# Optimization experiments

Hardware: AMD Instinct MI355X
Metric: run time of the kernel (lower is better)

Reference implementation:

```python
import jax, jax.numpy as jnp
import numpy as np

SIZE = 64          # node feature dim
T = 12             # num edge styles
N = 4000           # notes (nodes)
B = 1              # graph batch (torch branch requires B==1)
S2 = SIZE          # secondary_size == size (secondary_size=0 default)


def setup_inputs() -> dict:
    key = jax.random.key(0)
    ks = jax.random.split(key, 5)
    std_a = (2.0 / (S2 + S2)) ** 0.5
    std_b = (2.0 / (SIZE + S2)) ** 0.5
    std_c = (2.0 / (SIZE * T + S2)) ** 0.5
    x = jax.random.normal(ks[0], (B, N, SIZE), jnp.float32)
    # dense per-edge-type adjacency; scaled so repeated propagation stays bounded
    edge_matrix = jax.random.normal(ks[1], (T, N, N), jnp.float32) / np.float32(np.sqrt(N))
    ba = jnp.zeros((T, SIZE), jnp.float32)
    bw = jnp.zeros((3 * S2,), jnp.float32)
    wz_wr_wh = std_c * jax.random.normal(ks[2], (T, SIZE, 3 * S2), jnp.float32)
    uz_ur = std_b * jax.random.normal(ks[3], (SIZE, 2 * S2), jnp.float32)
    uh = std_a * jax.random.normal(ks[4], (S2, S2), jnp.float32)
    return dict(x=x, edge_matrix=edge_matrix, ba=ba, bw=bw,
                wz_wr_wh=wz_wr_wh, uz_ur=uz_ur, uh=uh, iteration=10)


def reference(x, edge_matrix, ba, bw, wz_wr_wh, uz_ur, uh, iteration):
    h = x  # [B, N, S]
    for _ in range(iteration):
        # per-edge-type propagation: edge_matrix[t].T @ h  -> [B, T, N, S]
        act = jnp.einsum('tnm,bns->btms', edge_matrix, h) + ba[None, :, None, :]
        # fused z/r/h projection per edge type: [B, T, N, 3*S2]
        awzrh = jnp.einsum('btms,tsk->btmk', act, wz_wr_wh) + bw
        awz, awr, awh = jnp.split(awzrh, 3, axis=-1)
        awz = awz.sum(1)  # sum over edge types -> [B, N, S2]
        awr = awr.sum(1)
        awh = awh.sum(1)
        uzr = h @ uz_ur                      # [B, N, 2*S2]
        uz, ur = jnp.split(uzr, 2, axis=-1)
        z = jax.nn.sigmoid(awz + uz)
        r = jax.nn.sigmoid(awr + ur)
        hh = jnp.tanh(awh + (r * h) @ uh)    # secondary_size == size branch
        h = (1.0 - z) * h + z * hh
    return h
```

## Files before the change

kernel.cpp:

```cpp
#include <hip/hip_runtime.h>
#include <stdint.h>

#define NN 4000
#define SD 64
#define TT 12
#define NITER 10
#define KP 4032
#define NKB 63
#define NMT 63

typedef _Float16 f16;
typedef _Float16 f16x8 __attribute__((ext_vector_type(8)));
typedef float    f32x4 __attribute__((ext_vector_type(4)));

__device__ __forceinline__ void dma16(const void* g, void* l) {
    __builtin_amdgcn_global_load_lds(
        (const __attribute__((address_space(1))) uint32_t*)g,
        (__attribute__((address_space(3))) uint32_t*)l, 16, 0, 0);
}

__global__ void wconv_kernel(const float* __restrict__ w, f16* __restrict__ wt) {
    int idx = blockIdx.x * 256 + threadIdx.x;
    if (idx >= TT * SD * 192) return;
    int t = idx / (SD * 192);
    int rem = idx - t * SD * 192;
    int s = rem / 192;
    int j = rem - s * 192;
    wt[t * 192 * 64 + j * 64 + (((s >> 3) ^ (j & 7)) << 3) + (s & 7)] = (f16)w[idx];
}

__global__ void init_kernel(const float* __restrict__ x, float* __restrict__ h32,
                            f16* __restrict__ hTb) {
    int idx = blockIdx.x * 256 + threadIdx.x;
    if (idx < NN * SD) h32[idx] = x[idx];
    if (idx < NKB * 64 * 64) {
        int row = idx >> 6;
        int s   = row & 63;
        int kb  = row >> 6;
        int p   = idx & 63;
        int pc  = p >> 3, pos = p & 7;
        int kk  = ((pc ^ (s & 7)) << 3) + pos;
        int n   = kb * 64 + kk;
        hTb[idx] = (n < NN) ? (f16)x[n * SD + s] : (f16)0.f;
    }
}

__global__ __launch_bounds__(256) void econv_kernel(const float* __restrict__ E,
                                                    f16* __restrict__ Ec) {
    __shared__ f16 lsT[64][72];
    const int mt = blockIdx.x, kb = blockIdx.y, t = blockIdx.z;
    const int tid = threadIdx.x;
    const int kr0 = tid >> 4;
    const int mc  = (tid & 15) << 2;
    const int gmb = mt * 64 + mc;
    #pragma unroll
    for (int p = 0; p < 4; ++p) {
        int kr = kr0 + p * 16;
        int k  = kb * 64 + kr;
        float4 v = {0.f, 0.f, 0.f, 0.f};
        if (k < NN) {
            const float* src = E + ((size_t)t * NN + k) * NN + gmb;
            if (gmb + 3 < NN) v = *(const float4*)src;
            else {
                if (gmb + 0 < NN) v.x = src[0];
                if (gmb + 1 < NN) v.y = src[1];
                if (gmb + 2 < NN) v.z = src[2];
                if (gmb + 3 < NN) v.w = src[3];
            }
        }
        lsT[mc + 0][kr] = (f16)v.x;
        lsT[mc + 1][kr] = (f16)v.y;
        lsT[mc + 2][kr] = (f16)v.z;
        lsT[mc + 3][kr] = (f16)v.w;
    }
    __syncthreads();
    f16* dstb = Ec + ((size_t)(t * NKB + kb) * KP + mt * 64) * 64;
    #pragma unroll
    for (int p = 0; p < 2; ++p) {
        int m  = (tid >> 3) + p * 32;
        int kc = tid & 7;
        uint4 w = *(const uint4*)&lsT[m][kc * 8];
        *(uint4*)(dstb + m * 64 + ((kc ^ (m & 7)) << 3)) = w;
    }
}

__global__ __launch_bounds__(256, 4) void gemm_kernel(
        const f16*  __restrict__ Ec,
        const f16*  __restrict__ hTb,
        const float* __restrict__ ba,
        const f16*  __restrict__ Wt,
        float*      __restrict__ slab)
{
    __shared__ __align__(16) char arena[32768];

    const int t    = blockIdx.y;
    const int mi   = blockIdx.x;
    const int tid  = threadIdx.x;
    const int w    = tid >> 6;
    const int lane = tid & 63;
    const int l15  = lane & 15;
    const int quad = lane >> 4;
    const int rA   = w * 16 + l15;
    const int swz  = l15 & 7;

    const char*  Ag    = (const char*)(Ec + ((size_t)t * NKB * KP + (size_t)mi * 64) * 64);
    const char*  Bg    = (const char*)hTb;
    const size_t Astep = (size_t)KP * 64 * sizeof(f16);
    const int    wo    = w * 2048 + lane * 16;
    const int    wl    = w * 2048;

    dma16(Ag + wo,        arena + wl);
    dma16(Ag + wo + 1024, arena + wl + 1024);
    dma16(Bg + wo,        arena + 16384 + wl);
    dma16(Bg + wo + 1024, arena + 16384 + wl + 1024);

    f32x4 acc[4];
    #pragma unroll
    for (int si = 0; si < 4; ++si) { f32x4 z = {0.f,0.f,0.f,0.f}; acc[si] = z; }

    for (int kb = 0; kb < NKB; ++kb) {
        const int cur = kb & 1;
        if (kb + 1 < NKB) {
            const char* a = Ag + (size_t)(kb + 1) * Astep;
            const char* b = Bg + (size_t)(kb + 1) * 8192;
            const int nb  = (cur ^ 1) * 8192;
            dma16(a + wo,        arena + nb + wl);
            dma16(a + wo + 1024, arena + nb + wl + 1024);
            dma16(b + wo,        arena + 16384 + nb + wl);
            dma16(b + wo + 1024, arena + 16384 + nb + wl + 1024);
            __builtin_amdgcn_s_waitcnt(0x0F74);
        } else {
            __builtin_amdgcn_s_waitcnt(0x0F70);
        }
        __builtin_amdgcn_s_barrier();
        const f16* Ab = (const f16*)(arena + cur * 8192);
        const f16* Bb = (const f16*)(arena + 16384 + cur * 8192);
        #pragma unroll
        for (int kh = 0; kh < 2; ++kh) {
            const int cA = quad + kh * 4;
            const f16x8 af = *(const f16x8*)(Ab + rA * 64 + ((cA ^ swz) << 3));
            #pragma unroll
            for (int si = 0; si < 4; ++si) {
                const int rB = si * 16 + l15;
                const f16x8 bf = *(const f16x8*)(Bb + rB * 64 + ((cA ^ swz) << 3));
                acc[si] = __builtin_amdgcn_mfma_f32_16x16x32_f16(af, bf, acc[si], 0, 0, 0);
            }
        }
        __builtin_amdgcn_s_barrier();
    }

    {
        const char* Wg = (const char*)(Wt + (size_t)t * 192 * 64);
        #pragma unroll
        for (int i = 0; i < 6; ++i)
            dma16(Wg + w * 6144 + i * 1024 + lane * 16, arena + 8192 + w * 6144 + i * 1024);
    }
    const int mrow = w * 16 + quad * 4;
    f16* actb = (f16*)arena;
    #pragma unroll
    for (int si = 0; si < 4; ++si) {
        const float bav = ba[t * SD + si * 16 + l15];
        const int col = si * 16 + l15;
        const int cc  = col >> 3, pos = col & 7;
        #pragma unroll
        for (int r = 0; r < 4; ++r) {
            const int m = mrow + r;
            actb[m * 64 + (((cc ^ (m & 7)) << 3)) + pos] = (f16)(acc[si][r] + bav);
        }
    }
    __syncthreads();

    f32x4 acc2[12];
    #pragma unroll
    for (int jf = 0; jf < 12; ++jf) { f32x4 z = {0.f,0.f,0.f,0.f}; acc2[jf] = z; }
    const f16* Wl = (const f16*)(arena + 8192);
    #pragma unroll
    for (int kh = 0; kh < 2; ++kh) {
        const int c2 = quad + kh * 4;
        const f16x8 a2 = *(const f16x8*)(actb + rA * 64 + ((c2 ^ swz) << 3));
        #pragma unroll
        for (int jf = 0; jf < 12; ++jf) {
            const int j = jf * 16 + l15;
            const f16x8 b2 = *(const f16x8*)(Wl + j * 64 + ((c2 ^ swz) << 3));
            acc2[jf] = __builtin_amdgcn_mfma_f32_16x16x32_f16(a2, b2, acc2[jf], 0, 0, 0);
        }
    }
    float* sb = slab + (size_t)t * NN * 192;
    #pragma unroll
    for (int jf = 0; jf < 12; ++jf) {
        #pragma unroll
        for (int r = 0; r < 4; ++r) {
            const int m = mi * 64 + mrow + r;
            if (m < NN)
                sb[(size_t)m * 192 + jf * 16 + l15] = acc2[jf][r];
        }
    }
}

__global__ __launch_bounds__(256) void gru_kernel(
        const float* __restrict__ slab, const float* __restrict__ bw,
        const float* __restrict__ uzur, const float* __restrict__ uhm,
        const float* __restrict__ hin, float* __restrict__ hout,
        f16* __restrict__ hTb) {
    __shared__ float uz_s[64][128];
    __shared__ float uh_s[64][65];
    __shared__ float h_s[32][65];
    __shared__ float uzr_s[32][130];
    __shared__ float rh_s[32][65];

    const int tid = threadIdx.x;
    const int n0  = blockIdx.x * 32;

    #pragma unroll
    for (int i = 0; i < 8; ++i) {
        int idx4 = tid + 256 * i;
        int k = idx4 >> 5;
        int c = (idx4 & 31) << 2;
        *(float4*)&uz_s[k][c] = *(const float4*)(uzur + (idx4 << 2));
    }
    #pragma unroll
    for (int i = 0; i < 4; ++i) {
        int idx4 = tid + 256 * i;
        int k = idx4 >> 4;
        int s = (idx4 & 15) << 2;
        float4 v = *(const float4*)(uhm + (idx4 << 2));
        uh_s[k][s] = v.x; uh_s[k][s+1] = v.y; uh_s[k][s+2] = v.z; uh_s[k][s+3] = v.w;
    }
    #pragma unroll
    for (int i = 0; i < 8; ++i) {
        int e = tid + 256 * i;
        int n = e >> 6, s = e & 63;
        h_s[n][s] = hin[(size_t)(n0 + n) * SD + s];
    }
    __syncthreads();

    {
        const int nd = tid & 31;
        const int c0 = (tid >> 5) << 4;
        float a[16];
        #pragma unroll
        for (int i = 0; i < 16; ++i) a[i] = 0.f;
        for (int k = 0; k < 64; ++k) {
            const float hv = h_s[nd][k];
            #pragma unroll
            for (int i = 0; i < 16; ++i) a[i] += hv * uz_s[k][c0 + i];
        }
        #pragma unroll
        for (int i = 0; i < 16; ++i) uzr_s[nd][c0 + i] = a[i];
    }
    __syncthreads();

    const int node = tid >> 3;
    const int sc   = (tid & 7) << 3;
    const int gn   = n0 + node;

    float az[8], ar[8], ah[8];
    #pragma unroll
    for (int i = 0; i < 8; ++i) { az[i] = 0.f; ar[i] = 0.f; ah[i] = 0.f; }
    for (int t = 0; t < TT; ++t) {
        const float* ab = slab + (size_t)t * NN * 192 + (size_t)gn * 192;
        float4 v;
        v = *(const float4*)(ab + sc);        az[0]+=v.x; az[1]+=v.y; az[2]+=v.z; az[3]+=v.w;
        v = *(const float4*)(ab + sc + 4);    az[4]+=v.x; az[5]+=v.y; az[6]+=v.z; az[7]+=v.w;
        v = *(const float4*)(ab + 64 + sc);   ar[0]+=v.x; ar[1]+=v.y; ar[2]+=v.z; ar[3]+=v.w;
        v = *(const float4*)(ab + 64 + sc+4); ar[4]+=v.x; ar[5]+=v.y; ar[6]+=v.z; ar[7]+=v.w;
        v = *(const float4*)(ab + 128 + sc);  ah[0]+=v.x; ah[1]+=v.y; ah[2]+=v.z; ah[3]+=v.w;
        v = *(const float4*)(ab + 128 + sc+4);ah[4]+=v.x; ah[5]+=v.y; ah[6]+=v.z; ah[7]+=v.w;
    }

    float z[8], r[8];
    #pragma unroll
    for (int i = 0; i < 8; ++i) {
        const float azv = az[i] + 12.f * bw[sc + i];
        const float arv = ar[i] + 12.f * bw[64 + sc + i];
        z[i] = 1.f / (1.f + __expf(-(azv + uzr_s[node][sc + i])));
        r[i] = 1.f / (1.f + __expf(-(arv + uzr_s[node][64 + sc + i])));
        rh_s[node][sc + i] = r[i] * h_s[node][sc + i];
    }
    __syncthreads();
    float a2[8];
    #pragma unroll
    for (int i = 0; i < 8; ++i) a2[i] = 0.f;
    for (int k = 0; k < 64; ++k) {
        const float rv = rh_s[node][k];
        #pragma unroll
        for (int i = 0; i < 8; ++i) a2[i] += rv * uh_s[k][sc + i];
    }
    const int kb = gn >> 6, kk = gn & 63;
    const int cc = kk >> 3, pos = kk & 7;
    #pragma unroll
    for (int i = 0; i < 8; ++i) {
        const float ahv = ah[i] + 12.f * bw[128 + sc + i];
        const float hh = tanhf(ahv + a2[i]);
        const float hv = h_s[node][sc + i];
        const float hn = (1.f - z[i]) * hv + z[i] * hh;
        const int s = sc + i;
        hout[(size_t)gn * SD + s] = hn;
        hTb[(size_t)(kb * 64 + s) * 64 + ((cc ^ (s & 7)) << 3) + pos] = (f16)hn;
    }
}

extern "C" void kernel_launch(void* const* d_in, const int* in_sizes, int n_in,
                              void* d_out, int out_size, void* d_ws, size_t ws_size,
                              hipStream_t stream) {
    const float* x    = (const float*)d_in[0];
    const float* E    = (const float*)d_in[1];
    const float* ba   = (const float*)d_in[2];
    const float* bw   = (const float*)d_in[3];
    const float* W    = (const float*)d_in[4];
    const float* uzur = (const float*)d_in[5];
    const float* uhm  = (const float*)d_in[6];
    float* out = (float*)d_out;

    char* ws = (char*)d_ws;
    float* h32  = (float*)(ws);
    f16*   hTb  = (f16*)(ws + (1 << 20));
    f16*   Wt   = (f16*)(ws + (1 << 20) + (1 << 19));
    float* slab = (float*)(ws + (2 << 20));
    f16*   Ec   = (f16*)(ws + (size_t)41943040);

    wconv_kernel<<<dim3(576), dim3(256), 0, stream>>>(W, Wt);
    init_kernel<<<dim3(1008), dim3(256), 0, stream>>>(x, h32, hTb);
    econv_kernel<<<dim3(NMT, NKB, TT), dim3(256), 0, stream>>>(E, Ec);
    for (int it = 0; it < NITER; ++it) {
        gemm_kernel<<<dim3(NMT, TT), dim3(256), 0, stream>>>(Ec, hTb, ba, Wt, slab);
        float* ho = (it == NITER - 1) ? out : h32;
        gru_kernel<<<dim3(125), dim3(256), 0, stream>>>(slab, bw, uzur, uhm, h32, ho, hTb);
    }
}
```

Before: 2.171 ms.

## Triple-buffer GEMM K-loop prefetch and halve GRU nodes per block

The GEMM main loop moves from a double-buffered LDS pipeline to a three-stage ring. Tiles for k+1 and k+2 are in flight while tile k is computed, with vmcnt waits tuned to retire only the oldest tile, to better hide global-to-LDS latency on the streamed adjacency. LDS per block grows to 48KB and occupancy is lowered to 3 blocks per CU. Separately, the GRU kernel processes 16 nodes per block instead of 32, doubling the grid to 250 blocks for better CU coverage. It also reuses the Uz/Ur LDS buffer for r*h to save shared memory.

```diff
diff --git a/kernel.cpp b/kernel.cpp
--- a/kernel.cpp
+++ b/kernel.cpp
@@ -84,14 +84,14 @@
     }
 }
 
-__global__ __launch_bounds__(256, 4) void gemm_kernel(
+__global__ __launch_bounds__(256, 3) void gemm_kernel(
         const f16*  __restrict__ Ec,
         const f16*  __restrict__ hTb,
         const float* __restrict__ ba,
         const f16*  __restrict__ Wt,
         float*      __restrict__ slab)
 {
-    __shared__ __align__(16) char arena[32768];
+    __shared__ __align__(16) char arena[49152];
 
     const int t    = blockIdx.y;
     const int mi   = blockIdx.x;
@@ -109,32 +109,21 @@
     const int    wo    = w * 2048 + lane * 16;
     const int    wl    = w * 2048;
 
-    dma16(Ag + wo,        arena + wl);
-    dma16(Ag + wo + 1024, arena + wl + 1024);
-    dma16(Bg + wo,        arena + 16384 + wl);
-    dma16(Bg + wo + 1024, arena + 16384 + wl + 1024);
-
     f32x4 acc[4];
     #pragma unroll
     for (int si = 0; si < 4; ++si) { f32x4 z = {0.f,0.f,0.f,0.f}; acc[si] = z; }
 
-    for (int kb = 0; kb < NKB; ++kb) {
-        const int cur = kb & 1;
-        if (kb + 1 < NKB) {
-            const char* a = Ag + (size_t)(kb + 1) * Astep;
-            const char* b = Bg + (size_t)(kb + 1) * 8192;
-            const int nb  = (cur ^ 1) * 8192;
-            dma16(a + wo,        arena + nb + wl);
-            dma16(a + wo + 1024, arena + nb + wl + 1024);
-            dma16(b + wo,        arena + 16384 + nb + wl);
-            dma16(b + wo + 1024, arena + 16384 + nb + wl + 1024);
-            __builtin_amdgcn_s_waitcnt(0x0F74);
-        } else {
-            __builtin_amdgcn_s_waitcnt(0x0F70);
-        }
-        __builtin_amdgcn_s_barrier();
-        const f16* Ab = (const f16*)(arena + cur * 8192);
-        const f16* Bb = (const f16*)(arena + 16384 + cur * 8192);
+    auto issue_tile = [&](int kbn, int cb) {
+        const char* a = Ag + (size_t)kbn * Astep;
+        const char* b = Bg + (size_t)kbn * 8192;
+        dma16(a + wo,        arena + cb * 8192 + wl);
+        dma16(a + wo + 1024, arena + cb * 8192 + wl + 1024);
+        dma16(b + wo,        arena + 24576 + cb * 8192 + wl);
+        dma16(b + wo + 1024, arena + 24576 + cb * 8192 + wl + 1024);
+    };
+    auto compute_tile = [&](int cb) {
+        const f16* Ab = (const f16*)(arena + cb * 8192);
+        const f16* Bb = (const f16*)(arena + 24576 + cb * 8192);
         #pragma unroll
         for (int kh = 0; kh < 2; ++kh) {
             const int cA = quad + kh * 4;
@@ -146,14 +135,41 @@
                 acc[si] = __builtin_amdgcn_mfma_f32_16x16x32_f16(af, bf, acc[si], 0, 0, 0);
             }
         }
+    };
+
+    issue_tile(0, 0);
+    issue_tile(1, 1);
+    issue_tile(2, 2);
+
+    int cbuf = 0;
+    for (int kb = 0; kb < 60; ++kb) {
+        __builtin_amdgcn_s_waitcnt(0x0F78);
         __builtin_amdgcn_s_barrier();
-    }
+        compute_tile(cbuf);
+        __builtin_amdgcn_s_barrier();
+        issue_tile(kb + 3, cbuf);
+        cbuf = (cbuf == 2) ? 0 : cbuf + 1;
+    }
+    __builtin_amdgcn_s_waitcnt(0x0F78);
+    __builtin_amdgcn_s_barrier();
+    compute_tile(cbuf);
+    __builtin_amdgcn_s_barrier();
+    cbuf = (cbuf == 2) ? 0 : cbuf + 1;
+    __builtin_amdgcn_s_waitcnt(0x0F74);
+    __builtin_amdgcn_s_barrier();
+    compute_tile(cbuf);
+    __builtin_amdgcn_s_barrier();
+    cbuf = (cbuf == 2) ? 0 : cbuf + 1;
+    __builtin_amdgcn_s_waitcnt(0x0F70);
+    __builtin_amdgcn_s_barrier();
+    compute_tile(cbuf);
+    __builtin_amdgcn_s_barrier();
 
     {
         const char* Wg = (const char*)(Wt + (size_t)t * 192 * 64);
         #pragma unroll
         for (int i = 0; i < 6; ++i)
-            dma16(Wg + w * 6144 + i * 1024 + lane * 16, arena + 8192 + w * 6144 + i * 1024);
+            dma16(Wg + w * 6144 + i * 1024 + lane * 16, arena + 24576 + w * 6144 + i * 1024);
     }
     const int mrow = w * 16 + quad * 4;
     f16* actb = (f16*)arena;
@@ -173,7 +189,7 @@
     f32x4 acc2[12];
     #pragma unroll
     for (int jf = 0; jf < 12; ++jf) { f32x4 z = {0.f,0.f,0.f,0.f}; acc2[jf] = z; }
-    const f16* Wl = (const f16*)(arena + 8192);
+    const f16* Wl = (const f16*)(arena + 24576);
     #pragma unroll
     for (int kh = 0; kh < 2; ++kh) {
         const int c2 = quad + kh * 4;
@@ -204,12 +220,12 @@
         f16* __restrict__ hTb) {
     __shared__ float uz_s[64][128];
     __shared__ float uh_s[64][65];
-    __shared__ float h_s[32][65];
-    __shared__ float uzr_s[32][130];
-    __shared__ float rh_s[32][65];
+    __shared__ float h_s[16][65];
+    __shared__ float uzr_s[16][130];
+    float (*rh_s)[65] = reinterpret_cast<float(*)[65]>(&uz_s[0][0]);
 
     const int tid = threadIdx.x;
-    const int n0  = blockIdx.x * 32;
+    const int n0  = blockIdx.x * 16;
 
     #pragma unroll
     for (int i = 0; i < 8; ++i) {
@@ -227,7 +243,7 @@
         uh_s[k][s] = v.x; uh_s[k][s+1] = v.y; uh_s[k][s+2] = v.z; uh_s[k][s+3] = v.w;
     }
     #pragma unroll
-    for (int i = 0; i < 8; ++i) {
+    for (int i = 0; i < 4; ++i) {
         int e = tid + 256 * i;
         int n = e >> 6, s = e & 63;
         h_s[n][s] = hin[(size_t)(n0 + n) * SD + s];
@@ -235,42 +251,40 @@
     __syncthreads();
 
     {
-        const int nd = tid & 31;
-        const int c0 = (tid >> 5) << 4;
-        float a[16];
-        #pragma unroll
-        for (int i = 0; i < 16; ++i) a[i] = 0.f;
+        const int nd = tid & 15;
+        const int c0 = (tid >> 4) << 3;
+        float a[8];
+        #pragma unroll
+        for (int i = 0; i < 8; ++i) a[i] = 0.f;
         for (int k = 0; k < 64; ++k) {
             const float hv = h_s[nd][k];
             #pragma unroll
-            for (int i = 0; i < 16; ++i) a[i] += hv * uz_s[k][c0 + i];
-        }
-        #pragma unroll
-        for (int i = 0; i < 16; ++i) uzr_s[nd][c0 + i] = a[i];
-    }
-    __syncthreads();
-
-    const int node = tid >> 3;
-    const int sc   = (tid & 7) << 3;
+            for (int i = 0; i < 8; ++i) a[i] += hv * uz_s[k][c0 + i];
+        }
+        #pragma unroll
+        for (int i = 0; i < 8; ++i) uzr_s[nd][c0 + i] = a[i];
+    }
+    __syncthreads();
+
+    const int node = tid >> 4;
+    const int sc   = (tid & 15) << 2;
     const int gn   = n0 + node;
 
-    float az[8], ar[8], ah[8];
-    #pragma unroll
-    for (int i = 0; i < 8; ++i) { az[i] = 0.f; ar[i] = 0.f; ah[i] = 0.f; }
+    float az[4], ar[4], ah[4];
+    #pragma unroll
+    for (int i = 0; i < 4; ++i) { az[i] = 0.f; ar[i] = 0.f; ah[i] = 0.f; }
+    #pragma unroll
     for (int t = 0; t < TT; ++t) {
         const float* ab = slab + (size_t)t * NN * 192 + (size_t)gn * 192;
         float4 v;
         v = *(const float4*)(ab + sc);        az[0]+=v.x; az[1]+=v.y; az[2]+=v.z; az[3]+=v.w;
-        v = *(const float4*)(ab + sc + 4);    az[4]+=v.x; az[5]+=v.y; az[6]+=v.z; az[7]+=v.w;
         v = *(const float4*)(ab + 64 + sc);   ar[0]+=v.x; ar[1]+=v.y; ar[2]+=v.z; ar[3]+=v.w;
-        v = *(const float4*)(ab + 64 + sc+4); ar[4]+=v.x; ar[5]+=v.y; ar[6]+=v.z; ar[7]+=v.w;
         v = *(const float4*)(ab + 128 + sc);  ah[0]+=v.x; ah[1]+=v.y; ah[2]+=v.z; ah[3]+=v.w;
-        v = *(const float4*)(ab + 128 + sc+4);ah[4]+=v.x; ah[5]+=v.y; ah[6]+=v.z; ah[7]+=v.w;
-    }
-
-    float z[8], r[8];
-    #pragma unroll
-    for (int i = 0; i < 8; ++i) {
+    }
+
+    float z[4], r[4];
+    #pragma unroll
+    for (int i = 0; i < 4; ++i) {
         const float azv = az[i] + 12.f * bw[sc + i];
         const float arv = ar[i] + 12.f * bw[64 + sc + i];
         z[i] = 1.f / (1.f + __expf(-(azv + uzr_s[node][sc + i])));
@@ -278,18 +292,18 @@
         rh_s[node][sc + i] = r[i] * h_s[node][sc + i];
     }
     __syncthreads();
-    float a2[8];
-    #pragma unroll
-    for (int i = 0; i < 8; ++i) a2[i] = 0.f;
+    float a2[4];
+    #pragma unroll
+    for (int i = 0; i < 4; ++i) a2[i] = 0.f;
     for (int k = 0; k < 64; ++k) {
         const float rv = rh_s[node][k];
         #pragma unroll
-        for (int i = 0; i < 8; ++i) a2[i] += rv * uh_s[k][sc + i];
+        for (int i = 0; i < 4; ++i) a2[i] += rv * uh_s[k][sc + i];
     }
     const int kb = gn >> 6, kk = gn & 63;
     const int cc = kk >> 3, pos = kk & 7;
     #pragma unroll
-    for (int i = 0; i < 8; ++i) {
+    for (int i = 0; i < 4; ++i) {
         const float ahv = ah[i] + 12.f * bw[128 + sc + i];
         const float hh = tanhf(ahv + a2[i]);
         const float hv = h_s[node][sc + i];
@@ -325,6 +339,6 @@
     for (int it = 0; it < NITER; ++it) {
         gemm_kernel<<<dim3(NMT, TT), dim3(256), 0, stream>>>(Ec, hTb, ba, Wt, slab);
         float* ho = (it == NITER - 1) ? out : h32;
-        gru_kernel<<<dim3(125), dim3(256), 0, stream>>>(slab, bw, uzur, uhm, h32, ho, hTb);
-    }
-}
+        gru_kernel<<<dim3(125 * 2), dim3(256), 0, stream>>>(slab, bw, uzur, uhm, h32, ho, hTb);
+    }
+}
```

After: 1.965 ms. 9.5% less time.

## Load GEMM operands directly from global into registers, reblock Ec, shrink GRU blocks

Applied to the files above, without the earlier changes.

The GEMM main loop no longer stages A and B tiles through LDS with async DMA and barriers. Each lane now loads its MFMA fragments straight from global memory, with a one-step register prefetch of A. To make those per-lane reads contiguous, Ec is reordered into contiguous 64x64 tiles per (t, mi) and the XOR swizzles on Ec and hTb are dropped. The GRU kernel is retiled to 8 nodes per block with 500 blocks to spread across more CUs, and its rh buffer is aliased onto the uz_s LDS region. The trade-off is more redundant global/L2 traffic for B across waves and blocks, with no LDS reuse, plus occupancy lowered to 3 blocks.

```diff
diff --git a/kernel.cpp b/kernel.cpp
--- a/kernel.cpp
+++ b/kernel.cpp
@@ -37,9 +37,7 @@
         int row = idx >> 6;
         int s   = row & 63;
         int kb  = row >> 6;
-        int p   = idx & 63;
-        int pc  = p >> 3, pos = p & 7;
-        int kk  = ((pc ^ (s & 7)) << 3) + pos;
+        int kk  = idx & 63;
         int n   = kb * 64 + kk;
         hTb[idx] = (n < NN) ? (f16)x[n * SD + s] : (f16)0.f;
     }
@@ -74,17 +72,17 @@
         lsT[mc + 3][kr] = (f16)v.w;
     }
     __syncthreads();
-    f16* dstb = Ec + ((size_t)(t * NKB + kb) * KP + mt * 64) * 64;
+    f16* dstb = Ec + (size_t)((t * NMT + mt) * NKB + kb) * 4096;
     #pragma unroll
     for (int p = 0; p < 2; ++p) {
         int m  = (tid >> 3) + p * 32;
         int kc = tid & 7;
         uint4 w = *(const uint4*)&lsT[m][kc * 8];
-        *(uint4*)(dstb + m * 64 + ((kc ^ (m & 7)) << 3)) = w;
-    }
-}
-
-__global__ __launch_bounds__(256, 4) void gemm_kernel(
+        *(uint4*)(dstb + m * 64 + (kc << 3)) = w;
+    }
+}
+
+__global__ __launch_bounds__(256, 3) void gemm_kernel(
         const f16*  __restrict__ Ec,
         const f16*  __restrict__ hTb,
         const float* __restrict__ ba,
@@ -103,50 +101,40 @@
     const int rA   = w * 16 + l15;
     const int swz  = l15 & 7;
 
-    const char*  Ag    = (const char*)(Ec + ((size_t)t * NKB * KP + (size_t)mi * 64) * 64);
-    const char*  Bg    = (const char*)hTb;
-    const size_t Astep = (size_t)KP * 64 * sizeof(f16);
-    const int    wo    = w * 2048 + lane * 16;
-    const int    wl    = w * 2048;
-
-    dma16(Ag + wo,        arena + wl);
-    dma16(Ag + wo + 1024, arena + wl + 1024);
-    dma16(Bg + wo,        arena + 16384 + wl);
-    dma16(Bg + wo + 1024, arena + 16384 + wl + 1024);
+    const f16* Arow = Ec + (size_t)(t * NMT + mi) * NKB * 4096 + rA * 64 + quad * 8;
+    const f16* Bbas = hTb + l15 * 64 + quad * 8;
 
     f32x4 acc[4];
     #pragma unroll
     for (int si = 0; si < 4; ++si) { f32x4 z = {0.f,0.f,0.f,0.f}; acc[si] = z; }
 
+    f16x8 aN0 = *(const f16x8*)(Arow);
+    f16x8 aN1 = *(const f16x8*)(Arow + 32);
+
+    #pragma unroll 1
     for (int kb = 0; kb < NKB; ++kb) {
-        const int cur = kb & 1;
-        if (kb + 1 < NKB) {
-            const char* a = Ag + (size_t)(kb + 1) * Astep;
-            const char* b = Bg + (size_t)(kb + 1) * 8192;
-            const int nb  = (cur ^ 1) * 8192;
-            dma16(a + wo,        arena + nb + wl);
-            dma16(a + wo + 1024, arena + nb + wl + 1024);
-            dma16(b + wo,        arena + 16384 + nb + wl);
-            dma16(b + wo + 1024, arena + 16384 + nb + wl + 1024);
-            __builtin_amdgcn_s_waitcnt(0x0F74);
-        } else {
-            __builtin_amdgcn_s_waitcnt(0x0F70);
-        }
-        __builtin_amdgcn_s_barrier();
-        const f16* Ab = (const f16*)(arena + cur * 8192);
-        const f16* Bb = (const f16*)(arena + 16384 + cur * 8192);
-        #pragma unroll
-        for (int kh = 0; kh < 2; ++kh) {
-            const int cA = quad + kh * 4;
-            const f16x8 af = *(const f16x8*)(Ab + rA * 64 + ((cA ^ swz) << 3));
-            #pragma unroll
-            for (int si = 0; si < 4; ++si) {
-                const int rB = si * 16 + l15;
-                const f16x8 bf = *(const f16x8*)(Bb + rB * 64 + ((cA ^ swz) << 3));
-                acc[si] = __builtin_amdgcn_mfma_f32_16x16x32_f16(af, bf, acc[si], 0, 0, 0);
-            }
-        }
-        __builtin_amdgcn_s_barrier();
+        const f16x8 a0 = aN0;
+        const f16x8 a1 = aN1;
+        const int kn = (kb < NKB - 1) ? kb + 1 : kb;
+        aN0 = *(const f16x8*)(Arow + kn * 4096);
+        aN1 = *(const f16x8*)(Arow + kn * 4096 + 32);
+        const f16* Bp = Bbas + (size_t)kb * 4096;
+        f16x8 b00 = *(const f16x8*)(Bp + 0 * 1024);
+        f16x8 b10 = *(const f16x8*)(Bp + 1 * 1024);
+        f16x8 b20 = *(const f16x8*)(Bp + 2 * 1024);
+        f16x8 b30 = *(const f16x8*)(Bp + 3 * 1024);
+        f16x8 b01 = *(const f16x8*)(Bp + 0 * 1024 + 32);
+        f16x8 b11 = *(const f16x8*)(Bp + 1 * 1024 + 32);
+        f16x8 b21 = *(const f16x8*)(Bp + 2 * 1024 + 32);
+        f16x8 b31 = *(const f16x8*)(Bp + 3 * 1024 + 32);
+        acc[0] = __builtin_amdgcn_mfma_f32_16x16x32_f16(a0, b00, acc[0], 0, 0, 0);
+        acc[1] = __builtin_amdgcn_mfma_f32_16x16x32_f16(a0, b10, acc[1], 0, 0, 0);
+        acc[2] = __builtin_amdgcn_mfma_f32_16x16x32_f16(a0, b20, acc[2], 0, 0, 0);
+        acc[3] = __builtin_amdgcn_mfma_f32_16x16x32_f16(a0, b30, acc[3], 0, 0, 0);
+        acc[0] = __builtin_amdgcn_mfma_f32_16x16x32_f16(a1, b01, acc[0], 0, 0, 0);
+        acc[1] = __builtin_amdgcn_mfma_f32_16x16x32_f16(a1, b11, acc[1], 0, 0, 0);
+        acc[2] = __builtin_amdgcn_mfma_f32_16x16x32_f16(a1, b21, acc[2], 0, 0, 0);
+        acc[3] = __builtin_amdgcn_mfma_f32_16x16x32_f16(a1, b31, acc[3], 0, 0, 0);
     }
 
     {
@@ -204,12 +192,12 @@
         f16* __restrict__ hTb) {
     __shared__ float uz_s[64][128];
     __shared__ float uh_s[64][65];
-    __shared__ float h_s[32][65];
-    __shared__ float uzr_s[32][130];
-    __shared__ float rh_s[32][65];
+    __shared__ float h_s[8][65];
+    __shared__ float uzr_s[8][130];
+    float (*rh_s)[65] = reinterpret_cast<float(*)[65]>(&uz_s[0][0]);
 
     const int tid = threadIdx.x;
-    const int n0  = blockIdx.x * 32;
+    const int n0  = blockIdx.x * 8;
 
     #pragma unroll
     for (int i = 0; i < 8; ++i) {
@@ -227,7 +215,7 @@
         uh_s[k][s] = v.x; uh_s[k][s+1] = v.y; uh_s[k][s+2] = v.z; uh_s[k][s+3] = v.w;
     }
     #pragma unroll
-    for (int i = 0; i < 8; ++i) {
+    for (int i = 0; i < 2; ++i) {
         int e = tid + 256 * i;
         int n = e >> 6, s = e & 63;
         h_s[n][s] = hin[(size_t)(n0 + n) * SD + s];
@@ -235,42 +223,40 @@
     __syncthreads();
 
     {
-        const int nd = tid & 31;
-        const int c0 = (tid >> 5) << 4;
-        float a[16];
-        #pragma unroll
-        for (int i = 0; i < 16; ++i) a[i] = 0.f;
+        const int nd = tid & 7;
+        const int c0 = (tid >> 3) << 2;
+        float a[4];
+        #pragma unroll
+        for (int i = 0; i < 4; ++i) a[i] = 0.f;
         for (int k = 0; k < 64; ++k) {
             const float hv = h_s[nd][k];
             #pragma unroll
-            for (int i = 0; i < 16; ++i) a[i] += hv * uz_s[k][c0 + i];
-        }
-        #pragma unroll
-        for (int i = 0; i < 16; ++i) uzr_s[nd][c0 + i] = a[i];
-    }
-    __syncthreads();
-
-    const int node = tid >> 3;
-    const int sc   = (tid & 7) << 3;
+            for (int i = 0; i < 4; ++i) a[i] += hv * uz_s[k][c0 + i];
+        }
+        #pragma unroll
+        for (int i = 0; i < 4; ++i) uzr_s[nd][c0 + i] = a[i];
+    }
+    __syncthreads();
+
+    const int node = tid >> 5;
+    const int sc   = (tid & 31) << 1;
     const int gn   = n0 + node;
 
-    float az[8], ar[8], ah[8];
-    #pragma unroll
-    for (int i = 0; i < 8; ++i) { az[i] = 0.f; ar[i] = 0.f; ah[i] = 0.f; }
+    float az[2], ar[2], ah[2];
+    #pragma unroll
+    for (int i = 0; i < 2; ++i) { az[i] = 0.f; ar[i] = 0.f; ah[i] = 0.f; }
+    #pragma unroll
     for (int t = 0; t < TT; ++t) {
         const float* ab = slab + (size_t)t * NN * 192 + (size_t)gn * 192;
-        float4 v;
-        v = *(const float4*)(ab + sc);        az[0]+=v.x; az[1]+=v.y; az[2]+=v.z; az[3]+=v.w;
-        v = *(const float4*)(ab + sc + 4);    az[4]+=v.x; az[5]+=v.y; az[6]+=v.z; az[7]+=v.w;
-        v = *(const float4*)(ab + 64 + sc);   ar[0]+=v.x; ar[1]+=v.y; ar[2]+=v.z; ar[3]+=v.w;
-        v = *(const float4*)(ab + 64 + sc+4); ar[4]+=v.x; ar[5]+=v.y; ar[6]+=v.z; ar[7]+=v.w;
-        v = *(const float4*)(ab + 128 + sc);  ah[0]+=v.x; ah[1]+=v.y; ah[2]+=v.z; ah[3]+=v.w;
-        v = *(const float4*)(ab + 128 + sc+4);ah[4]+=v.x; ah[5]+=v.y; ah[6]+=v.z; ah[7]+=v.w;
-    }
-
-    float z[8], r[8];
-    #pragma unroll
-    for (int i = 0; i < 8; ++i) {
+        float2 v;
+        v = *(const float2*)(ab + sc);        az[0]+=v.x; az[1]+=v.y;
+        v = *(const float2*)(ab + 64 + sc);   ar[0]+=v.x; ar[1]+=v.y;
+        v = *(const float2*)(ab + 128 + sc);  ah[0]+=v.x; ah[1]+=v.y;
+    }
+
+    float z[2], r[2];
+    #pragma unroll
+    for (int i = 0; i < 2; ++i) {
         const float azv = az[i] + 12.f * bw[sc + i];
         const float arv = ar[i] + 12.f * bw[64 + sc + i];
         z[i] = 1.f / (1.f + __expf(-(azv + uzr_s[node][sc + i])));
@@ -278,25 +264,24 @@
         rh_s[node][sc + i] = r[i] * h_s[node][sc + i];
     }
     __syncthreads();
-    float a2[8];
-    #pragma unroll
-    for (int i = 0; i < 8; ++i) a2[i] = 0.f;
+    float a2[2];
+    #pragma unroll
+    for (int i = 0; i < 2; ++i) a2[i] = 0.f;
     for (int k = 0; k < 64; ++k) {
         const float rv = rh_s[node][k];
         #pragma unroll
-        for (int i = 0; i < 8; ++i) a2[i] += rv * uh_s[k][sc + i];
+        for (int i = 0; i < 2; ++i) a2[i] += rv * uh_s[k][sc + i];
     }
     const int kb = gn >> 6, kk = gn & 63;
-    const int cc = kk >> 3, pos = kk & 7;
-    #pragma unroll
-    for (int i = 0; i < 8; ++i) {
+    #pragma unroll
+    for (int i = 0; i < 2; ++i) {
         const float ahv = ah[i] + 12.f * bw[128 + sc + i];
         const float hh = tanhf(ahv + a2[i]);
         const float hv = h_s[node][sc + i];
         const float hn = (1.f - z[i]) * hv + z[i] * hh;
         const int s = sc + i;
         hout[(size_t)gn * SD + s] = hn;
-        hTb[(size_t)(kb * 64 + s) * 64 + ((cc ^ (s & 7)) << 3) + pos] = (f16)hn;
+        hTb[(size_t)(kb * 64 + s) * 64 + kk] = (f16)hn;
     }
 }
 
@@ -325,6 +310,6 @@
     for (int it = 0; it < NITER; ++it) {
         gemm_kernel<<<dim3(NMT, TT), dim3(256), 0, stream>>>(Ec, hTb, ba, Wt, slab);
         float* ho = (it == NITER - 1) ? out : h32;
-        gru_kernel<<<dim3(125), dim3(256), 0, stream>>>(slab, bw, uzur, uhm, h32, ho, hTb);
-    }
-}
+        gru_kernel<<<dim3(500), dim3(256), 0, stream>>>(slab, bw, uzur, uhm, h32, ho, hTb);
+    }
+}
```

New measurement: 3.281 ms. +51.1%, slower.
